# Performance work log

Hardware: AMD Instinct MI355X
Metric: run time of the kernel (lower is better)

The kernel has to match this reference:

```python
import jax, jax.numpy as jnp
import numpy as np

B, TOK, D, H, L = 64, 20, 512, 8, 4
S = 512          # tokens per half
HD = D // H
ODIM = 32        # encoder_output_dim


def _ln(x, g, b):
    m = x.mean(-1, keepdims=True)
    v = ((x - m) ** 2).mean(-1, keepdims=True)
    return (x - m) / jnp.sqrt(v + 1e-5) * g + b


def _alibi_slopes(h):
    # mirrors FlashAttentionBlock.build_alibi_slopes (base=2.0)
    base = 2.0
    return jnp.asarray([1.0 / base ** (i // (h // base)) for i in range(h)], dtype=jnp.float32)


def setup_inputs() -> dict:
    key = jax.random.key(0)
    ks = jax.random.split(key, 16)
    r = lambda i, shape, s=0.02: jax.random.normal(ks[i], shape, jnp.float32) * s
    return {
        'x': jax.random.normal(ks[0], (B, 2 * S * TOK), jnp.float32),
        'in_W': r(1, (TOK, D)), 'in_b': jnp.zeros((D,)),
        'qkv_W': r(2, (L, D, 3 * D)), 'qkv_b': jnp.zeros((L, 3 * D)),
        'ln1_g': jnp.ones((L, D)), 'ln1_b': jnp.zeros((L, D)),
        'ffn_W1': r(3, (L, D, 4 * D)), 'ffn_b1': jnp.zeros((L, 4 * D)),
        'ffn_W2': r(4, (L, 4 * D, D)), 'ffn_b2': jnp.zeros((L, D)),
        'ln2_g': jnp.ones((L, D)), 'ln2_b': jnp.zeros((L, D)),
        'out_W': r(5, (D, ODIM)), 'out_b': jnp.zeros((ODIM,)),
        'd1_W': r(6, (2 * S * ODIM, 256)), 'd1_b': jnp.zeros((256,)),
        'bn1_g': jnp.ones((256,)), 'bn1_b': jnp.zeros((256,)),
        'bn1_m': jnp.zeros((256,)), 'bn1_v': jnp.ones((256,)),
        'd2_W': r(7, (256, 128)), 'd2_b': jnp.zeros((128,)),
        'bn2_g': jnp.ones((128,)), 'bn2_b': jnp.zeros((128,)),
        'bn2_m': jnp.zeros((128,)), 'bn2_v': jnp.ones((128,)),
        'fin_W': r(8, (128, 1)), 'fin_b': jnp.zeros((1,)),
    }


def _forward(x, in_W, in_b, qkv_W, qkv_b, ln1_g, ln1_b, ffn_W1, ffn_b1,
             ffn_W2, ffn_b2, ln2_g, ln2_b, out_W, out_b,
             d1_W, d1_b, bn1_g, bn1_b, bn1_m, bn1_v,
             d2_W, d2_b, bn2_g, bn2_b, bn2_m, bn2_v, fin_W, fin_b):
    slopes = _alibi_slopes(H)                                   # [H]
    pos = jnp.arange(S)
    # non-causal ALiBi bias: -slope * |i - j|, shape [H, S, S]
    bias = -slopes[:, None, None] * jnp.abs(pos[:, None] - pos[None, :]).astype(jnp.float32)
    scale = 1.0 / np.sqrt(HD).astype(np.float32)

    def encode(xh):
        b = xh.shape[0]
        t = xh.reshape(b, S, TOK) @ in_W + in_b                 # [b, S, D]
        for l in range(L):
            res = t
            qkv = (t @ qkv_W[l] + qkv_b[l]).reshape(b, S, 3, H, HD)
            q, k, v = qkv[:, :, 0], qkv[:, :, 1], qkv[:, :, 2]  # [b, S, H, HD]
            scores = jnp.einsum('bqhd,bkhd->bhqk', q, k) * scale + bias[None]
            attn = jax.nn.softmax(scores, axis=-1)
            o = jnp.einsum('bhqk,bkhd->bqhd', attn, v).reshape(b, S, D)
            t = _ln(res + o, ln1_g[l], ln1_b[l])
            res = t
            f = jax.nn.relu(t @ ffn_W1[l] + ffn_b1[l]) @ ffn_W2[l] + ffn_b2[l]
            t = _ln(res + f, ln2_g[l], ln2_b[l])
        return (t @ out_W + out_b).reshape(b, -1)               # [b, S*ODIM]

    half = S * TOK
    h = jnp.concatenate([encode(x[:, :half]), encode(x[:, half:])], axis=-1)
    bn = lambda z, g, bb, m, v: (z - m) / jnp.sqrt(v + 1e-5) * g + bb
    h = bn(jax.nn.relu(h @ d1_W + d1_b), bn1_g, bn1_b, bn1_m, bn1_v)
    h = bn(jax.nn.relu(h @ d2_W + d2_b), bn2_g, bn2_b, bn2_m, bn2_v)
    return (h @ fin_W + fin_b).squeeze(-1)                      # [B]


def reference(x, in_W, in_b, qkv_W, qkv_b, ln1_g, ln1_b, ffn_W1, ffn_b1,
              ffn_W2, ffn_b2, ln2_g, ln2_b, out_W, out_b,
              d1_W, d1_b, bn1_g, bn1_b, bn1_m, bn1_v,
              d2_W, d2_b, bn2_g, bn2_b, bn2_m, bn2_v, fin_W, fin_b):
    return _forward(x, in_W, in_b, qkv_W, qkv_b, ln1_g, ln1_b, ffn_W1, ffn_b1,
                    ffn_W2, ffn_b2, ln2_g, ln2_b, out_W, out_b,
                    d1_W, d1_b, bn1_g, bn1_b, bn1_m, bn1_v,
                    d2_W, d2_b, bn2_g, bn2_b, bn2_m, bn2_v, fin_W, fin_b)
```

## Files before the change

### kernel.cpp

```cpp
#include <hip/hip_runtime.h>

#define DEV __device__ __forceinline__

using bf16x8 = __attribute__((ext_vector_type(8))) __bf16;
using f32x4  = __attribute__((ext_vector_type(4))) float;
using u16x8  = __attribute__((ext_vector_type(8))) unsigned short;

DEV unsigned short f2bf(float f) {
  unsigned u = __builtin_bit_cast(unsigned, f);
  u += 0x7fffu + ((u >> 16) & 1u);
  return (unsigned short)(u >> 16);
}
DEV float bf2f(unsigned short h) {
  unsigned u = ((unsigned)h) << 16;
  return __builtin_bit_cast(float, u);
}
DEV f32x4 mfma16(u16x8 a, u16x8 b, f32x4 c) {
  return __builtin_amdgcn_mfma_f32_16x16x32_bf16(
      __builtin_bit_cast(bf16x8, a), __builtin_bit_cast(bf16x8, b), c, 0, 0, 0);
}
DEV f32x4 zero4() { f32x4 z = {0.f, 0.f, 0.f, 0.f}; return z; }

DEV void glds16(const unsigned short* g, unsigned short* l) {
  __builtin_amdgcn_global_load_lds(
      (const __attribute__((address_space(1))) unsigned int*)g,
      (__attribute__((address_space(3))) unsigned int*)l, 16, 0, 0);
}

enum { EPI_BIAS = 0, EPI_RELU = 1, EPI_OUT = 2 };

template <int EPI>
__global__ __launch_bounds__(512, 2) void gemm256_k(
    const unsigned short* __restrict__ A, const unsigned short* __restrict__ Bt,
    const float* __restrict__ bias, unsigned short* __restrict__ C, int N, int K) {
  __shared__ unsigned short As[2][8192];
  __shared__ unsigned short Bs[2][8192];
  const int tid = threadIdx.x;
  const int lane = tid & 63, wv = tid >> 6;
  const int q = lane >> 4, ln = lane & 15;
  const int wr = wv >> 2, wc = wv & 3;

  const int Nt = gridDim.x, Mt = gridDim.y;
  const int lin = blockIdx.x + Nt * blockIdx.y;
  const int xcd = lin & 7;
  const int j = lin >> 3;
  const int mi = xcd * (Mt >> 3) + j / Nt;
  const int ni = j % Nt;
  const int m0 = mi << 8, n0 = ni << 8;

  f32x4 acc[8][4];
#pragma unroll
  for (int i = 0; i < 8; ++i)
#pragma unroll
    for (int jj = 0; jj < 4; ++jj) acc[i][jj] = zero4();

  const int srow = wv * 16 + (lane >> 2);
  const int scol = (((lane & 3) ^ ((lane >> 3) & 3)) << 3);
  const unsigned short* Ap = A + (size_t)(m0 + srow) * K + scol;
  const unsigned short* Bp = Bt + (size_t)(n0 + srow) * K + scol;

  auto STAGE = [&](int buf, int kb) {
    unsigned short* ab = &As[buf][wv * 512];
    unsigned short* bb = &Bs[buf][wv * 512];
    glds16(Ap + kb, ab);
    glds16(Ap + (size_t)128 * K + kb, ab + 4096);
    glds16(Bp + kb, bb);
    glds16(Bp + (size_t)128 * K + kb, bb + 4096);
  };

  const int sw = ((q ^ ((ln >> 1) & 3)) << 3);
  const int NTt = K >> 5;

  STAGE(0, 0);
  if (NTt > 1) {
    STAGE(1, 32);
    asm volatile("s_waitcnt vmcnt(4)" ::: "memory");
  } else {
    asm volatile("s_waitcnt vmcnt(0)" ::: "memory");
  }
  __builtin_amdgcn_sched_barrier(0);
  __builtin_amdgcn_s_barrier();
  __builtin_amdgcn_sched_barrier(0);

  for (int t = 0; t < NTt; ++t) {
    const int cur = t & 1;
    u16x8 af[4], bf[4], ag[4];
#pragma unroll
    for (int mt = 0; mt < 4; ++mt)
      af[mt] = *(const u16x8*)(&As[cur][(wr * 128 + mt * 16 + ln) * 32 + sw]);
#pragma unroll
    for (int nt = 0; nt < 4; ++nt)
      bf[nt] = *(const u16x8*)(&Bs[cur][(wc * 64 + nt * 16 + ln) * 32 + sw]);
    __builtin_amdgcn_s_setprio(1);
#pragma unroll
    for (int nt = 0; nt < 4; ++nt)
#pragma unroll
      for (int mt = 0; mt < 4; ++mt) acc[mt][nt] = mfma16(af[mt], bf[nt], acc[mt][nt]);
    __builtin_amdgcn_s_setprio(0);
#pragma unroll
    for (int mt = 0; mt < 4; ++mt)
      ag[mt] = *(const u16x8*)(&As[cur][(wr * 128 + (mt + 4) * 16 + ln) * 32 + sw]);
    asm volatile("s_waitcnt lgkmcnt(0)" ::: "memory");
    __builtin_amdgcn_sched_barrier(0);
    __builtin_amdgcn_s_barrier();
    __builtin_amdgcn_sched_barrier(0);
    if (t + 2 < NTt) STAGE(cur, (t + 2) * 32);
    __builtin_amdgcn_s_setprio(1);
#pragma unroll
    for (int nt = 0; nt < 4; ++nt)
#pragma unroll
      for (int mt = 0; mt < 4; ++mt)
        acc[mt + 4][nt] = mfma16(ag[mt], bf[nt], acc[mt + 4][nt]);
    __builtin_amdgcn_s_setprio(0);
    if (t < NTt - 1) {
      if (t + 2 < NTt) {
        asm volatile("s_waitcnt vmcnt(4)" ::: "memory");
      } else {
        asm volatile("s_waitcnt vmcnt(0)" ::: "memory");
      }
      __builtin_amdgcn_sched_barrier(0);
      __builtin_amdgcn_s_barrier();
      __builtin_amdgcn_sched_barrier(0);
    }
  }

#pragma unroll
  for (int mt = 0; mt < 8; ++mt) {
    const int rowb = m0 + wr * 128 + mt * 16 + q * 4;
#pragma unroll
    for (int nt = 0; nt < 4; ++nt) {
      const int col = n0 + wc * 64 + nt * 16 + ln;
      const float bs = bias[col];
#pragma unroll
      for (int r = 0; r < 4; ++r) {
        float v = acc[mt][nt][r] + bs;
        if (EPI == EPI_RELU) v = fmaxf(v, 0.f);
        C[(size_t)(rowb + r) * N + col] = f2bf(v);
      }
    }
  }
}

template <int EPI>
__global__ __launch_bounds__(256) void gemm_k(
    const unsigned short* __restrict__ A, const unsigned short* __restrict__ Bt,
    const float* __restrict__ bias, unsigned short* __restrict__ C, int N, int K) {
  __shared__ unsigned short As[128 * 64];
  __shared__ unsigned short Bs[128 * 64];
  const int tid = threadIdx.x;
  const int lane = tid & 63, wv = tid >> 6;
  const int q = lane >> 4, ln = lane & 15;
  const int wr = wv >> 1, wc = wv & 1;

  const int Nt = gridDim.x, Mt = gridDim.y;
  const int lin = blockIdx.x + Nt * blockIdx.y;
  const int xcd = lin & 7;
  const int j = lin >> 3;
  const int mi = xcd * (Mt >> 3) + j / Nt;
  const int ni = j % Nt;
  const int m0 = mi << 7, n0 = ni << 7;

  f32x4 acc[4][4];
#pragma unroll
  for (int i = 0; i < 4; ++i)
#pragma unroll
    for (int jj = 0; jj < 4; ++jj) acc[i][jj] = zero4();

  const int ra = lane >> 3;
  const int ca = ((lane & 7) ^ ra) << 3;
  const unsigned short* Ap = A + (size_t)(m0 + wv * 32 + ra) * K + ca;
  const unsigned short* Bp = Bt + (size_t)(n0 + wv * 32 + ra) * K + ca;
  unsigned short* AsW = As + wv * 2048;
  unsigned short* BsW = Bs + wv * 2048;
  const int ln7 = ln & 7;

  for (int kb = 0; kb < K; kb += 64) {
    __syncthreads();
#pragma unroll
    for (int t = 0; t < 4; ++t) {
      glds16(Ap + (size_t)(t * 8) * K + kb, AsW + t * 512);
      glds16(Bp + (size_t)(t * 8) * K + kb, BsW + t * 512);
    }
    __syncthreads();
#pragma unroll
    for (int kk = 0; kk < 2; ++kk) {
      const int c = kk * 4 + q;
      const int lo = ln * 64 + ((c ^ ln7) << 3);
      u16x8 af[4];
#pragma unroll
      for (int mt = 0; mt < 4; ++mt)
        af[mt] = *(const u16x8*)(As + (wr * 64 + mt * 16) * 64 + lo);
#pragma unroll
      for (int nt = 0; nt < 4; ++nt) {
        u16x8 bf = *(const u16x8*)(Bs + (wc * 64 + nt * 16) * 64 + lo);
#pragma unroll
        for (int mt = 0; mt < 4; ++mt) acc[mt][nt] = mfma16(af[mt], bf, acc[mt][nt]);
      }
    }
  }

#pragma unroll
  for (int mt = 0; mt < 4; ++mt) {
    const int rowb = m0 + wr * 64 + mt * 16 + q * 4;
#pragma unroll
    for (int nt = 0; nt < 4; ++nt) {
      const int col = n0 + wc * 64 + nt * 16 + ln;
      if (EPI == EPI_OUT && col >= 32) continue;
      const float bs = bias[col];
      const int ldc = (EPI == EPI_OUT) ? 32 : N;
#pragma unroll
      for (int r = 0; r < 4; ++r) {
        float v = acc[mt][nt][r] + bs;
        if (EPI == EPI_RELU) v = fmaxf(v, 0.f);
        C[(size_t)(rowb + r) * ldc + col] = f2bf(v);
      }
    }
  }
}

__global__ __launch_bounds__(256) void vt_k(const unsigned short* __restrict__ big,
                                            unsigned short* __restrict__ vt) {
  __shared__ unsigned short td[64 * 72];
  const int tid = threadIdx.x;
  const int sh = blockIdx.x;
  const int seq = sh >> 3, h = sh & 7;
  const int kt = blockIdx.y;
  {
    const int key = tid >> 2, hdc = (tid & 3) << 4;
    const unsigned short* src =
        big + ((size_t)seq * 512 + kt * 64 + key) * 1536 + 1024 + h * 64 + hdc;
    *(u16x8*)(td + key * 72 + hdc) = *(const u16x8*)src;
    *(u16x8*)(td + key * 72 + hdc + 8) = *(const u16x8*)(src + 8);
  }
  __syncthreads();
  {
    const int hd = tid >> 2, kc = (tid & 3) << 4;
    u16x8 a, b;
#pragma unroll
    for (int j = 0; j < 8; ++j) a[j] = td[(kc + j) * 72 + hd];
#pragma unroll
    for (int j = 0; j < 8; ++j) b[j] = td[(kc + 8 + j) * 72 + hd];
    unsigned short* dst = vt + ((size_t)sh * 64 + hd) * 512 + kt * 64 + kc;
    *(u16x8*)dst = a;
    *(u16x8*)(dst + 8) = b;
  }
}

__global__ __launch_bounds__(256) void attn_k(const unsigned short* __restrict__ qkv,
                                              const unsigned short* __restrict__ vt,
                                              unsigned short* __restrict__ o) {
  __shared__ unsigned short Qs[128 * 72];
  __shared__ unsigned short Ks[64 * 72];
  __shared__ unsigned short Vts[64 * 72];
  __shared__ unsigned short Ps[128 * 72];
  const int tid = threadIdx.x;
  const int lane = tid & 63, w = tid >> 6, q = lane >> 4, ln = lane & 15;
  const int bh = blockIdx.x;
  const int seq = bh >> 3, h = bh & 7;
  const int qt = blockIdx.y;
  const size_t tokb = (size_t)seq * 512;
  const int qoff = h * 64, koff = 512 + h * 64;
  const float c1 = 0.125f * 1.44269504f;
  const float c2 = ((h < 4) ? 1.0f : 0.5f) * 1.44269504f;

#pragma unroll
  for (int p = 0; p < 4; ++p) {
    int c = p * 256 + tid;
    int row = c >> 3, cc = (c & 7) << 3;
    u16x8 v = *(const u16x8*)(qkv + (tokb + qt * 128 + row) * 1536 + qoff + cc);
    *(u16x8*)(Qs + row * 72 + cc) = v;
  }
  __syncthreads();
  u16x8 aq[2][2];
#pragma unroll
  for (int mt = 0; mt < 2; ++mt)
#pragma unroll
    for (int kc = 0; kc < 2; ++kc)
      aq[mt][kc] = *(const u16x8*)(Qs + (w * 32 + mt * 16 + ln) * 72 + kc * 32 + q * 8);

  float lacc[2][4];
  f32x4 o_acc[2][4];
#pragma unroll
  for (int mt = 0; mt < 2; ++mt)
#pragma unroll
    for (int r = 0; r < 4; ++r) lacc[mt][r] = 0.f;
#pragma unroll
  for (int mt = 0; mt < 2; ++mt)
#pragma unroll
    for (int ht = 0; ht < 4; ++ht) o_acc[mt][ht] = zero4();

  const int krow = tid >> 3, kcc = (tid & 7) << 3;
  const int vhd = tid >> 2, vc = (tid & 3) << 4;
  const unsigned short* vbase = vt + ((size_t)bh * 64 + vhd) * 512 + vc;

  for (int kt = 0; kt < 8; ++kt) {
    __syncthreads();
    {
      u16x8 v0 = *(const u16x8*)(qkv + (tokb + kt * 64 + krow) * 1536 + koff + kcc);
      u16x8 v1 = *(const u16x8*)(qkv + (tokb + kt * 64 + krow + 32) * 1536 + koff + kcc);
      *(u16x8*)(Ks + krow * 72 + kcc) = v0;
      *(u16x8*)(Ks + (krow + 32) * 72 + kcc) = v1;
      u16x8 w0 = *(const u16x8*)(vbase + kt * 64);
      u16x8 w1 = *(const u16x8*)(vbase + kt * 64 + 8);
      *(u16x8*)(Vts + vhd * 72 + vc) = w0;
      *(u16x8*)(Vts + vhd * 72 + vc + 8) = w1;
    }
    __syncthreads();

    f32x4 sacc[2][4];
#pragma unroll
    for (int mt = 0; mt < 2; ++mt)
#pragma unroll
      for (int nt = 0; nt < 4; ++nt) sacc[mt][nt] = zero4();
#pragma unroll
    for (int nt = 0; nt < 4; ++nt)
#pragma unroll
      for (int kc = 0; kc < 2; ++kc) {
        u16x8 bk = *(const u16x8*)(Ks + (nt * 16 + ln) * 72 + kc * 32 + q * 8);
#pragma unroll
        for (int mt = 0; mt < 2; ++mt) sacc[mt][nt] = mfma16(aq[mt][kc], bk, sacc[mt][nt]);
      }

    const float kbase = (float)(kt * 64 + ln);
#pragma unroll
    for (int mt = 0; mt < 2; ++mt) {
      const float qpb = (float)(qt * 128 + w * 32 + mt * 16 + q * 4);
#pragma unroll
      for (int nt = 0; nt < 4; ++nt) {
        const float kp = kbase + (float)(nt * 16);
#pragma unroll
        for (int r = 0; r < 4; ++r) {
          const float ad = fabsf(qpb + (float)r - kp);
          const float p = exp2f(fmaf(sacc[mt][nt][r], c1, -c2 * ad));
          const unsigned u = __builtin_bit_cast(unsigned, p);
          const unsigned short pb = (unsigned short)((u + 0x8000u) >> 16);
          Ps[(w * 32 + mt * 16 + q * 4 + r) * 72 + nt * 16 + ln] = pb;
          lacc[mt][r] += bf2f(pb);
        }
      }
    }
#pragma unroll
    for (int kc = 0; kc < 2; ++kc) {
      u16x8 pa[2];
#pragma unroll
      for (int mt = 0; mt < 2; ++mt)
        pa[mt] = *(const u16x8*)(Ps + (w * 32 + mt * 16 + ln) * 72 + kc * 32 + q * 8);
#pragma unroll
      for (int ht = 0; ht < 4; ++ht) {
        u16x8 bv = *(const u16x8*)(Vts + (ht * 16 + ln) * 72 + kc * 32 + q * 8);
#pragma unroll
        for (int mt = 0; mt < 2; ++mt) o_acc[mt][ht] = mfma16(pa[mt], bv, o_acc[mt][ht]);
      }
    }
  }

  float rl[2][4];
#pragma unroll
  for (int mt = 0; mt < 2; ++mt)
#pragma unroll
    for (int r = 0; r < 4; ++r) {
      float l = lacc[mt][r];
#pragma unroll
      for (int msk = 1; msk < 16; msk <<= 1) l += __shfl_xor(l, msk, 64);
      rl[mt][r] = 1.0f / l;
    }

#pragma unroll
  for (int mt = 0; mt < 2; ++mt)
#pragma unroll
    for (int ht = 0; ht < 4; ++ht)
#pragma unroll
      for (int r = 0; r < 4; ++r) {
        const int row = qt * 128 + w * 32 + mt * 16 + q * 4 + r;
        const float val = o_acc[mt][ht][r] * rl[mt][r];
        o[(tokb + row) * 512 + h * 64 + ht * 16 + ln] = f2bf(val);
      }
}

__global__ __launch_bounds__(256) void ln_k(const unsigned short* res,
                                            const unsigned short* __restrict__ y,
                                            const float* __restrict__ g,
                                            const float* __restrict__ b,
                                            unsigned short* out) {
  const int lane = threadIdx.x & 63, wv = threadIdx.x >> 6;
  const size_t row = (size_t)blockIdx.x * 4 + wv;
  const size_t base = row * 512 + lane * 8;
  u16x8 rv = *(const u16x8*)(res + base);
  u16x8 yv = *(const u16x8*)(y + base);
  float v[8];
  float s = 0.f, s2 = 0.f;
#pragma unroll
  for (int i = 0; i < 8; ++i) {
    v[i] = bf2f(rv[i]) + bf2f(yv[i]);
    s += v[i];
    s2 += v[i] * v[i];
  }
#pragma unroll
  for (int m = 1; m < 64; m <<= 1) {
    s += __shfl_xor(s, m, 64);
    s2 += __shfl_xor(s2, m, 64);
  }
  const float mean = s * (1.f / 512.f);
  const float var = s2 * (1.f / 512.f) - mean * mean;
  const float rstd = rsqrtf(var + 1e-5f);
  const int c = lane * 8;
  u16x8 ov;
#pragma unroll
  for (int i = 0; i < 8; ++i) ov[i] = f2bf((v[i] - mean) * rstd * g[c + i] + b[c + i]);
  *(u16x8*)(out + base) = ov;
}

__global__ __launch_bounds__(256) void transpose_w(const float* __restrict__ in,
                                                   unsigned short* __restrict__ out,
                                                   int Kin, int Nin, int Kout, int Nout) {
  __shared__ float tile[32][33];
  const int nb = blockIdx.x * 32, kb = blockIdx.y * 32;
  const int tx = threadIdx.x & 31, ty = threadIdx.x >> 5;
#pragma unroll
  for (int i = 0; i < 32; i += 8) {
    int k = kb + ty + i, n = nb + tx;
    tile[ty + i][tx] = (k < Kin && n < Nin) ? in[(size_t)k * Nin + n] : 0.f;
  }
  __syncthreads();
#pragma unroll
  for (int i = 0; i < 32; i += 8) {
    int n = nb + ty + i, k = kb + tx;
    if (n < Nout && k < Kout) out[(size_t)n * Kout + k] = f2bf(tile[tx][ty + i]);
  }
}

__global__ __launch_bounds__(256) void xpad_k(const float* __restrict__ x,
                                              unsigned short* __restrict__ xp) {
  const int idx = blockIdx.x * 256 + threadIdx.x;
  const int tok = idx >> 6, k = idx & 63;
  const int seq = tok >> 9, s = tok & 511;
  const int hf = seq >> 6, b = seq & 63;
  float v = 0.f;
  if (k < 20) v = x[(size_t)b * 20480 + hf * 10240 + s * 20 + k];
  xp[idx] = f2bf(v);
}

__global__ __launch_bounds__(256) void d1_part(const unsigned short* __restrict__ enc,
                                               const float* __restrict__ W,
                                               float* __restrict__ pz) {
  __shared__ float ef[64 * 128];
  const int tid = threadIdx.x;
  const int kb = blockIdx.x * 128;
  const int hf = kb >> 14;
  const int j0 = kb & 16383;
  {
    const int m = tid >> 2, c = (tid & 3) * 32;
    const unsigned short* src = enc + (size_t)hf * 1048576 + (size_t)m * 16384 + j0 + c;
#pragma unroll
    for (int i = 0; i < 4; ++i) {
      u16x8 v = *(const u16x8*)(src + i * 8);
#pragma unroll
      for (int jj = 0; jj < 8; ++jj) ef[m * 128 + c + i * 8 + jj] = bf2f(v[jj]);
    }
  }
  __syncthreads();
  const int n = tid;
  float acc[64];
#pragma unroll
  for (int m = 0; m < 64; ++m) acc[m] = 0.f;
  for (int kc = 0; kc < 128; kc += 4) {
    const float w0 = W[(size_t)(kb + kc) * 256 + n];
    const float w1 = W[(size_t)(kb + kc + 1) * 256 + n];
    const float w2 = W[(size_t)(kb + kc + 2) * 256 + n];
    const float w3 = W[(size_t)(kb + kc + 3) * 256 + n];
#pragma unroll
    for (int m = 0; m < 64; ++m) {
      const f32x4 e = *(const f32x4*)(ef + m * 128 + kc);
      acc[m] += e[0] * w0 + e[1] * w1 + e[2] * w2 + e[3] * w3;
    }
  }
#pragma unroll
  for (int m = 0; m < 64; ++m)
    pz[(size_t)(blockIdx.x * 64 + m) * 256 + n] = acc[m];
}

__global__ __launch_bounds__(256) void d1_fin(const float* __restrict__ pz,
                                              const float* __restrict__ d1b,
                                              const float* __restrict__ g,
                                              const float* __restrict__ b,
                                              const float* __restrict__ mm,
                                              const float* __restrict__ vv,
                                              float* __restrict__ h1) {
  const int m = blockIdx.x, n = threadIdx.x;
  float a = d1b[n];
  for (int sl = 0; sl < 256; ++sl) a += pz[(size_t)(sl * 64 + m) * 256 + n];
  a = fmaxf(a, 0.f);
  a = (a - mm[n]) * rsqrtf(vv[n] + 1e-5f) * g[n] + b[n];
  h1[m * 256 + n] = a;
}

__global__ __launch_bounds__(128) void d2_k(const float* __restrict__ h1,
                                            const float* __restrict__ W,
                                            const float* __restrict__ bb,
                                            const float* __restrict__ g,
                                            const float* __restrict__ b,
                                            const float* __restrict__ mm,
                                            const float* __restrict__ vv,
                                            float* __restrict__ h2) {
  __shared__ float hs[256];
  const int m = blockIdx.x, n = threadIdx.x;
  hs[n] = h1[m * 256 + n];
  hs[n + 128] = h1[m * 256 + n + 128];
  __syncthreads();
  float a = bb[n];
#pragma unroll 8
  for (int k = 0; k < 256; ++k) a += hs[k] * W[k * 128 + n];
  a = fmaxf(a, 0.f);
  a = (a - mm[n]) * rsqrtf(vv[n] + 1e-5f) * g[n] + b[n];
  h2[m * 128 + n] = a;
}

__global__ __launch_bounds__(64) void fin_k(const float* __restrict__ h2,
                                            const float* __restrict__ W,
                                            const float* __restrict__ fb,
                                            float* __restrict__ out) {
  const int m = threadIdx.x;
  float a = fb[0];
#pragma unroll 8
  for (int k = 0; k < 128; ++k) a += h2[m * 128 + k] * W[k];
  out[m] = a;
}

extern "C" void kernel_launch(void* const* d_in, const int* in_sizes, int n_in,
                              void* d_out, int out_size, void* d_ws, size_t ws_size,
                              hipStream_t stream) {
  const float* x      = (const float*)d_in[0];
  const float* in_W   = (const float*)d_in[1];
  const float* in_b   = (const float*)d_in[2];
  const float* qkv_W  = (const float*)d_in[3];
  const float* qkv_b  = (const float*)d_in[4];
  const float* ln1_g  = (const float*)d_in[5];
  const float* ln1_b  = (const float*)d_in[6];
  const float* ffn_W1 = (const float*)d_in[7];
  const float* ffn_b1 = (const float*)d_in[8];
  const float* ffn_W2 = (const float*)d_in[9];
  const float* ffn_b2 = (const float*)d_in[10];
  const float* ln2_g  = (const float*)d_in[11];
  const float* ln2_b  = (const float*)d_in[12];
  const float* out_W  = (const float*)d_in[13];
  const float* out_b  = (const float*)d_in[14];
  const float* d1W    = (const float*)d_in[15];
  const float* d1b    = (const float*)d_in[16];
  const float* bn1g   = (const float*)d_in[17];
  const float* bn1b   = (const float*)d_in[18];
  const float* bn1m   = (const float*)d_in[19];
  const float* bn1v   = (const float*)d_in[20];
  const float* d2W    = (const float*)d_in[21];
  const float* d2b    = (const float*)d_in[22];
  const float* bn2g   = (const float*)d_in[23];
  const float* bn2b   = (const float*)d_in[24];
  const float* bn2m   = (const float*)d_in[25];
  const float* bn2v   = (const float*)d_in[26];
  const float* finW   = (const float*)d_in[27];
  const float* finb   = (const float*)d_in[28];
  (void)in_sizes; (void)n_in; (void)out_size; (void)ws_size;

  char* ws = (char*)d_ws;
  size_t off = 0;
  auto alloc = [&](size_t bytes) {
    char* p = ws + off;
    off += (bytes + 255) & ~(size_t)255;
    return p;
  };
  unsigned short* t     = (unsigned short*)alloc(32768ull * 512 * 2);
  unsigned short* big   = (unsigned short*)alloc(32768ull * 2048 * 2);
  unsigned short* ob    = (unsigned short*)alloc(32768ull * 512 * 2);
  unsigned short* xpad  = (unsigned short*)alloc(65536ull * 64 * 2);
  unsigned short* enc   = (unsigned short*)alloc(65536ull * 32 * 2);
  unsigned short* inWt  = (unsigned short*)alloc(512ull * 64 * 2);
  unsigned short* qkvWt = (unsigned short*)alloc(4ull * 1536 * 512 * 2);
  unsigned short* f1Wt  = (unsigned short*)alloc(4ull * 2048 * 512 * 2);
  unsigned short* f2Wt  = (unsigned short*)alloc(4ull * 512 * 2048 * 2);
  unsigned short* outWt = (unsigned short*)alloc(128ull * 512 * 2);
  float* h1 = (float*)alloc(64ull * 256 * 4);
  float* h2 = (float*)alloc(64ull * 128 * 4);
  float* pz = (float*)big;
  unsigned short* vtb = big + (size_t)32768 * 1536;

  xpad_k<<<16384, 256, 0, stream>>>(x, xpad);
  transpose_w<<<dim3(16, 2), 256, 0, stream>>>(in_W, inWt, 20, 512, 64, 512);
  transpose_w<<<dim3(4, 16), 256, 0, stream>>>(out_W, outWt, 512, 32, 512, 128);
  for (int l = 0; l < 4; ++l) {
    transpose_w<<<dim3(48, 16), 256, 0, stream>>>(qkv_W + (size_t)l * 512 * 1536,
                                                  qkvWt + (size_t)l * 1536 * 512, 512, 1536, 512, 1536);
    transpose_w<<<dim3(64, 16), 256, 0, stream>>>(ffn_W1 + (size_t)l * 512 * 2048,
                                                  f1Wt + (size_t)l * 2048 * 512, 512, 2048, 512, 2048);
    transpose_w<<<dim3(16, 64), 256, 0, stream>>>(ffn_W2 + (size_t)l * 2048 * 512,
                                                  f2Wt + (size_t)l * 512 * 2048, 2048, 512, 2048, 512);
  }

  for (int hf = 0; hf < 2; ++hf) {
    gemm256_k<EPI_BIAS><<<dim3(2, 128), 512, 0, stream>>>(xpad + (size_t)hf * 32768 * 64, inWt, in_b, t, 512, 64);
    for (int l = 0; l < 4; ++l) {
      gemm256_k<EPI_BIAS><<<dim3(6, 128), 512, 0, stream>>>(t, qkvWt + (size_t)l * 1536 * 512,
                                                            qkv_b + l * 1536, big, 1536, 512);
      vt_k<<<dim3(512, 8), 256, 0, stream>>>(big, vtb);
      attn_k<<<dim3(512, 4), 256, 0, stream>>>(big, vtb, ob);
      ln_k<<<8192, 256, 0, stream>>>(t, ob, ln1_g + l * 512, ln1_b + l * 512, t);
      gemm256_k<EPI_RELU><<<dim3(8, 128), 512, 0, stream>>>(t, f1Wt + (size_t)l * 2048 * 512,
                                                            ffn_b1 + l * 2048, big, 2048, 512);
      gemm256_k<EPI_BIAS><<<dim3(2, 128), 512, 0, stream>>>(big, f2Wt + (size_t)l * 512 * 2048,
                                                            ffn_b2 + l * 512, ob, 512, 2048);
      ln_k<<<8192, 256, 0, stream>>>(t, ob, ln2_g + l * 512, ln2_b + l * 512, t);
    }
    gemm_k<EPI_OUT><<<dim3(1, 256), 256, 0, stream>>>(t, outWt, out_b,
                                                      enc + (size_t)hf * 32768 * 32, 128, 512);
  }

  d1_part<<<256, 256, 0, stream>>>(enc, d1W, pz);
  d1_fin<<<64, 256, 0, stream>>>(pz, d1b, bn1g, bn1b, bn1m, bn1v, h1);
  d2_k<<<64, 128, 0, stream>>>(h1, d2W, d2b, bn2g, bn2b, bn2m, bn2v, h2);
  fin_k<<<1, 64, 0, stream>>>(h2, finW, finb, (float*)d_out);
}
```

Before: 3.295 ms.

## Load K/V tiles via direct global-to-LDS with XOR swizzle and transpose S

The attention kernel now fills K and V tiles with global_load_lds directly into unpadded, XOR-swizzled shared buffers, so the data no longer passes through registers. It also swaps the MFMA operands so each lane holds scores for a single query row, which allows packed 4-element P stores and a cheaper row-sum reduction. P reuses the Q buffer, which lowers LDS use and may raise occupancy. The risks are the correctness of the swizzle and the per-wave load mapping, and the P writes overwriting Q, which is only safe because Q is already in registers.

```diff
diff --git a/kernel.cpp b/kernel.cpp
--- a/kernel.cpp
+++ b/kernel.cpp
@@ -5,6 +5,7 @@
 using bf16x8 = __attribute__((ext_vector_type(8))) __bf16;
 using f32x4  = __attribute__((ext_vector_type(4))) float;
 using u16x8  = __attribute__((ext_vector_type(8))) unsigned short;
+using u16x4  = __attribute__((ext_vector_type(4))) unsigned short;
 
 DEV unsigned short f2bf(float f) {
   unsigned u = __builtin_bit_cast(unsigned, f);
@@ -250,9 +251,9 @@
                                               const unsigned short* __restrict__ vt,
                                               unsigned short* __restrict__ o) {
   __shared__ unsigned short Qs[128 * 72];
-  __shared__ unsigned short Ks[64 * 72];
-  __shared__ unsigned short Vts[64 * 72];
-  __shared__ unsigned short Ps[128 * 72];
+  __shared__ unsigned short Ks[64 * 64];
+  __shared__ unsigned short Vts[64 * 64];
+  unsigned short* Ps = Qs;
   const int tid = threadIdx.x;
   const int lane = tid & 63, w = tid >> 6, q = lane >> 4, ln = lane & 15;
   const int bh = blockIdx.x;
@@ -278,33 +279,27 @@
     for (int kc = 0; kc < 2; ++kc)
       aq[mt][kc] = *(const u16x8*)(Qs + (w * 32 + mt * 16 + ln) * 72 + kc * 32 + q * 8);
 
-  float lacc[2][4];
+  float lacc[2] = {0.f, 0.f};
   f32x4 o_acc[2][4];
 #pragma unroll
   for (int mt = 0; mt < 2; ++mt)
 #pragma unroll
-    for (int r = 0; r < 4; ++r) lacc[mt][r] = 0.f;
-#pragma unroll
-  for (int mt = 0; mt < 2; ++mt)
-#pragma unroll
     for (int ht = 0; ht < 4; ++ht) o_acc[mt][ht] = zero4();
 
-  const int krow = tid >> 3, kcc = (tid & 7) << 3;
-  const int vhd = tid >> 2, vc = (tid & 3) << 4;
-  const unsigned short* vbase = vt + ((size_t)bh * 64 + vhd) * 512 + vc;
+  const int sr = lane >> 3;
+  const int sc = ((lane & 7) ^ sr) << 3;
+  const unsigned short* Kp = qkv + (tokb + w * 16 + sr) * 1536 + koff + sc;
+  const unsigned short* Vp = vt + ((size_t)bh * 64 + w * 16 + sr) * 512 + sc;
+  unsigned short* KsW = Ks + w * 1024;
+  unsigned short* VsW = Vts + w * 1024;
+  const int ln7 = ln & 7;
 
   for (int kt = 0; kt < 8; ++kt) {
     __syncthreads();
-    {
-      u16x8 v0 = *(const u16x8*)(qkv + (tokb + kt * 64 + krow) * 1536 + koff + kcc);
-      u16x8 v1 = *(const u16x8*)(qkv + (tokb + kt * 64 + krow + 32) * 1536 + koff + kcc);
-      *(u16x8*)(Ks + krow * 72 + kcc) = v0;
-      *(u16x8*)(Ks + (krow + 32) * 72 + kcc) = v1;
-      u16x8 w0 = *(const u16x8*)(vbase + kt * 64);
-      u16x8 w1 = *(const u16x8*)(vbase + kt * 64 + 8);
-      *(u16x8*)(Vts + vhd * 72 + vc) = w0;
-      *(u16x8*)(Vts + vhd * 72 + vc + 8) = w1;
-    }
+    glds16(Kp + (size_t)(kt * 64) * 1536, KsW);
+    glds16(Kp + (size_t)(kt * 64 + 8) * 1536, KsW + 512);
+    glds16(Vp + kt * 64, VsW);
+    glds16(Vp + kt * 64 + (size_t)8 * 512, VsW + 512);
     __syncthreads();
 
     f32x4 sacc[2][4];
@@ -316,27 +311,30 @@
     for (int nt = 0; nt < 4; ++nt)
 #pragma unroll
       for (int kc = 0; kc < 2; ++kc) {
-        u16x8 bk = *(const u16x8*)(Ks + (nt * 16 + ln) * 72 + kc * 32 + q * 8);
-#pragma unroll
-        for (int mt = 0; mt < 2; ++mt) sacc[mt][nt] = mfma16(aq[mt][kc], bk, sacc[mt][nt]);
-      }
-
-    const float kbase = (float)(kt * 64 + ln);
+        u16x8 bk = *(const u16x8*)(Ks + (nt * 16 + ln) * 64 + (((kc * 4 + q) ^ ln7) << 3));
+#pragma unroll
+        for (int mt = 0; mt < 2; ++mt) sacc[mt][nt] = mfma16(bk, aq[mt][kc], sacc[mt][nt]);
+      }
+
+    const float qp0 = (float)(qt * 128 + w * 32 + ln);
+    const float kb0 = (float)(kt * 64 + q * 4);
 #pragma unroll
     for (int mt = 0; mt < 2; ++mt) {
-      const float qpb = (float)(qt * 128 + w * 32 + mt * 16 + q * 4);
+      const float qpm = qp0 + (float)(mt * 16);
 #pragma unroll
       for (int nt = 0; nt < 4; ++nt) {
-        const float kp = kbase + (float)(nt * 16);
+        const float kp = kb0 + (float)(nt * 16);
+        u16x4 pk;
 #pragma unroll
         for (int r = 0; r < 4; ++r) {
-          const float ad = fabsf(qpb + (float)r - kp);
+          const float ad = fabsf(qpm - (kp + (float)r));
           const float p = exp2f(fmaf(sacc[mt][nt][r], c1, -c2 * ad));
           const unsigned u = __builtin_bit_cast(unsigned, p);
           const unsigned short pb = (unsigned short)((u + 0x8000u) >> 16);
-          Ps[(w * 32 + mt * 16 + q * 4 + r) * 72 + nt * 16 + ln] = pb;
-          lacc[mt][r] += bf2f(pb);
+          pk[r] = pb;
+          lacc[mt] += bf2f(pb);
         }
+        *(u16x4*)(Ps + (w * 32 + mt * 16 + ln) * 72 + nt * 16 + q * 4) = pk;
       }
     }
 #pragma unroll
@@ -347,7 +345,7 @@
         pa[mt] = *(const u16x8*)(Ps + (w * 32 + mt * 16 + ln) * 72 + kc * 32 + q * 8);
 #pragma unroll
       for (int ht = 0; ht < 4; ++ht) {
-        u16x8 bv = *(const u16x8*)(Vts + (ht * 16 + ln) * 72 + kc * 32 + q * 8);
+        u16x8 bv = *(const u16x8*)(Vts + (ht * 16 + ln) * 64 + (((kc * 4 + q) ^ ln7) << 3));
 #pragma unroll
         for (int mt = 0; mt < 2; ++mt) o_acc[mt][ht] = mfma16(pa[mt], bv, o_acc[mt][ht]);
       }
@@ -356,14 +354,14 @@
 
   float rl[2][4];
 #pragma unroll
-  for (int mt = 0; mt < 2; ++mt)
-#pragma unroll
-    for (int r = 0; r < 4; ++r) {
-      float l = lacc[mt][r];
-#pragma unroll
-      for (int msk = 1; msk < 16; msk <<= 1) l += __shfl_xor(l, msk, 64);
-      rl[mt][r] = 1.0f / l;
-    }
+  for (int mt = 0; mt < 2; ++mt) {
+    float l = lacc[mt];
+    l += __shfl_xor(l, 16, 64);
+    l += __shfl_xor(l, 32, 64);
+    const int sb = (lane >> 4) * 20;
+#pragma unroll
+    for (int r = 0; r < 4; ++r) rl[mt][r] = 1.0f / __shfl(l, sb + r, 64);
+  }
 
 #pragma unroll
   for (int mt = 0; mt < 2; ++mt)
```

Result: faster. 3.226 ms (-2.1%).
